# Kernel optimization log

Hardware: AMD Instinct MI355X
Metric: run time of the kernel (lower is better)

## Reference

```python
import jax, jax.numpy as jnp
import numpy as np

B, NX, NY = 16, 1024, 1024
DIN_X, DIN_Y = 768, 283
DK, DV, NH = 80, 80, 8
HK, HV = DK // NH, DV // NH  # 10, 10
NORM = 1.0 / np.sqrt(HK)


def setup_inputs() -> dict:
    key = jax.random.key(0)
    kx, ky, kq, kk, kv = jax.random.split(key, 5)
    x = jax.random.normal(kx, (B, NX, DIN_X), dtype=jnp.float32)
    y = jax.random.normal(ky, (B, NY, DIN_Y), dtype=jnp.float32)
    attn_mask = jnp.zeros((B, NX, NY), dtype=jnp.float32)  # unused in forward (dead arg in original)
    # torch nn.Linear weights are [out, in]; kaiming-uniform-ish init scale
    Wq = jax.random.normal(kq, (DK, DIN_X), dtype=jnp.float32) / np.sqrt(DIN_X)
    Wk = jax.random.normal(kk, (DK, DIN_Y), dtype=jnp.float32) / np.sqrt(DIN_Y)
    Wv = jax.random.normal(kv, (DV, DIN_Y), dtype=jnp.float32) / np.sqrt(DIN_Y)
    return {"x": x, "y": y, "attn_mask": attn_mask, "Wq": Wq, "Wk": Wk, "Wv": Wv}


def reference(x, y, attn_mask, Wq, Wk, Wv):
    b, n_x, _ = x.shape
    n_y = y.shape[1]
    # projections (Linear, no bias): [B,N,D] @ W^T
    q = (x @ Wq.T).reshape(b, n_x, NH, HK).transpose(0, 2, 1, 3)  # [B,H,Nx,hk]
    k = (y @ Wk.T).reshape(b, n_y, NH, HK).transpose(0, 2, 1, 3)  # [B,H,Ny,hk]
    v = (y @ Wv.T).reshape(b, n_y, NH, HV).transpose(0, 2, 1, 3)  # [B,H,Ny,hv]
    scores = jnp.einsum("bhqd,bhkd->bhqk", q, k) * NORM          # [B,H,Nx,Ny]
    dist = jax.nn.softmax(scores, axis=-1)
    # dropout p=0.5 is identity in eval mode
    att = jnp.einsum("bhqk,bhkd->bhqd", dist, v)                  # [B,H,Nx,hv]
    att = att.transpose(0, 2, 1, 3).reshape(b, n_x, DV)           # [B,Nx,dim_v]
    return att, dist
```

## Files before the change

kernel.cpp:

```cpp
#include <hip/hip_runtime.h>
#include <hip/hip_bf16.h>

#define BB 16
#define NXX 1024
#define NYY 1024
#define DINX 768
#define DINY 283
#define NHH 8
#define HKK 10
#define DKV 80
#define NORMF 0.31622776601683794f

__global__ __launch_bounds__(256) void proj_kernel(
    const float* __restrict__ X, const float* __restrict__ W,
    float* __restrict__ Out, int Din) {
  const int LDP = 68;
  __shared__ float Xs[64 * LDP];
  __shared__ float Ws[80 * LDP];
  const int t = threadIdx.x;
  const int rb = blockIdx.x * 64;
  const int tc = t & 15;
  const int tr = t >> 4;

  float acc[4][5];
#pragma unroll
  for (int i = 0; i < 4; ++i)
#pragma unroll
    for (int j = 0; j < 5; ++j) acc[i][j] = 0.f;

  const int nchunk = (Din + 63) >> 6;
  for (int ch = 0; ch < nchunk; ++ch) {
    const int dk = ch << 6;
    __syncthreads();
#pragma unroll
    for (int i = 0; i < 16; ++i) {
      int idx = i * 256 + t;
      int r = idx >> 6, c = idx & 63;
      int d = dk + c;
      Xs[r * LDP + c] = (d < Din) ? X[(size_t)(rb + r) * Din + d] : 0.f;
    }
#pragma unroll
    for (int i = 0; i < 20; ++i) {
      int idx = i * 256 + t;
      int r = idx >> 6, c = idx & 63;
      int d = dk + c;
      Ws[r * LDP + c] = (d < Din) ? W[(size_t)r * Din + d] : 0.f;
    }
    __syncthreads();
#pragma unroll
    for (int dv = 0; dv < 16; ++dv) {
      float4 xv[4], wv[5];
#pragma unroll
      for (int i = 0; i < 4; ++i)
        xv[i] = *(const float4*)&Xs[(tr * 4 + i) * LDP + dv * 4];
#pragma unroll
      for (int j = 0; j < 5; ++j)
        wv[j] = *(const float4*)&Ws[(tc + 16 * j) * LDP + dv * 4];
#pragma unroll
      for (int i = 0; i < 4; ++i)
#pragma unroll
        for (int j = 0; j < 5; ++j) {
          acc[i][j] += xv[i].x * wv[j].x;
          acc[i][j] += xv[i].y * wv[j].y;
          acc[i][j] += xv[i].z * wv[j].z;
          acc[i][j] += xv[i].w * wv[j].w;
        }
    }
  }
#pragma unroll
  for (int i = 0; i < 4; ++i)
#pragma unroll
    for (int j = 0; j < 5; ++j)
      Out[(size_t)(rb + tr * 4 + i) * DKV + tc + 16 * j] = acc[i][j];
}

__global__ __launch_bounds__(256) void attn_kernel(
    const float* __restrict__ Qw, const float* __restrict__ Kw,
    const float* __restrict__ Vw, float* __restrict__ out_att,
    float* __restrict__ out_dist) {
  __shared__ float Ks[256 * 12];
  __shared__ float Vs[256 * 12];
  __shared__ float qs[256 * 12];
  __shared__ float rls[256];

  const int t = threadIdx.x;
  const int bid = blockIdx.x;
  const int qc = bid & 3;
  const int h = (bid >> 2) & 7;
  const int b = bid >> 5;

  const int qrow = qc * 256 + t;
  const size_t g = (size_t)b * NXX + qrow;

  float qr[10];
  {
    const float2* qp = (const float2*)(Qw + g * DKV + h * HKK);
#pragma unroll
    for (int dd = 0; dd < 5; ++dd) {
      float2 v = qp[dd];
      qr[2 * dd] = v.x * NORMF;
      qr[2 * dd + 1] = v.y * NORMF;
      *(float2*)&qs[t * 12 + 2 * dd] = make_float2(qr[2 * dd], qr[2 * dd + 1]);
    }
  }

  float acc[10];
#pragma unroll
  for (int d = 0; d < 10; ++d) acc[d] = 0.f;
  float l = 0.f;

  for (int kt = 0; kt < 4; ++kt) {
    __syncthreads();
    {
      const size_t gk = (size_t)b * NYY + kt * 256 + t;
      const float2* kp = (const float2*)(Kw + gk * DKV + h * HKK);
      const float2* vp = (const float2*)(Vw + gk * DKV + h * HKK);
#pragma unroll
      for (int dd = 0; dd < 5; ++dd) {
        *(float2*)&Ks[t * 12 + 2 * dd] = kp[dd];
        *(float2*)&Vs[t * 12 + 2 * dd] = vp[dd];
      }
    }
    __syncthreads();
#pragma unroll 2
    for (int kk = 0; kk < 256; ++kk) {
      float kf[10], vf[10];
      {
        float4 a0 = *(const float4*)&Ks[kk * 12];
        float4 a1 = *(const float4*)&Ks[kk * 12 + 4];
        float2 a2 = *(const float2*)&Ks[kk * 12 + 8];
        kf[0] = a0.x; kf[1] = a0.y; kf[2] = a0.z; kf[3] = a0.w;
        kf[4] = a1.x; kf[5] = a1.y; kf[6] = a1.z; kf[7] = a1.w;
        kf[8] = a2.x; kf[9] = a2.y;
        float4 b0 = *(const float4*)&Vs[kk * 12];
        float4 b1 = *(const float4*)&Vs[kk * 12 + 4];
        float2 b2 = *(const float2*)&Vs[kk * 12 + 8];
        vf[0] = b0.x; vf[1] = b0.y; vf[2] = b0.z; vf[3] = b0.w;
        vf[4] = b1.x; vf[5] = b1.y; vf[6] = b1.z; vf[7] = b1.w;
        vf[8] = b2.x; vf[9] = b2.y;
      }
      float s = 0.f;
#pragma unroll
      for (int d = 0; d < 10; ++d) s += qr[d] * kf[d];
      float p = __expf(s);
      l += p;
#pragma unroll
      for (int d = 0; d < 10; ++d) acc[d] += p * vf[d];
    }
  }

  const float rl = 1.0f / l;
  rls[t] = rl;
  {
    float* ap = out_att + g * DKV + h * HKK;
#pragma unroll
    for (int dd = 0; dd < 5; ++dd)
      *(float2*)&ap[2 * dd] = make_float2(acc[2 * dd] * rl, acc[2 * dd + 1] * rl);
  }
  __syncthreads();

  const size_t dbase = (((size_t)(b * NHH + h)) * NXX + qc * 256) * NYY;
  for (int kq = 0; kq < 4; ++kq) {
    const int k = kq * 256 + t;
    float kf[10];
    {
      const float2* kp = (const float2*)(Kw + ((size_t)b * NYY + k) * DKV + h * HKK);
#pragma unroll
      for (int dd = 0; dd < 5; ++dd) {
        float2 v = kp[dd];
        kf[2 * dd] = v.x;
        kf[2 * dd + 1] = v.y;
      }
    }
    float* dp = out_dist + dbase + k;
    for (int qq = 0; qq < 256; ++qq) {
      float4 a0 = *(const float4*)&qs[qq * 12];
      float4 a1 = *(const float4*)&qs[qq * 12 + 4];
      float2 a2 = *(const float2*)&qs[qq * 12 + 8];
      float s = kf[0] * a0.x + kf[1] * a0.y + kf[2] * a0.z + kf[3] * a0.w +
                kf[4] * a1.x + kf[5] * a1.y + kf[6] * a1.z + kf[7] * a1.w +
                kf[8] * a2.x + kf[9] * a2.y;
      dp[(size_t)qq * NYY] = __expf(s) * rls[qq];
    }
  }
}

extern "C" void kernel_launch(void* const* d_in, const int* in_sizes, int n_in,
                              void* d_out, int out_size, void* d_ws, size_t ws_size,
                              hipStream_t stream) {
  (void)in_sizes; (void)n_in; (void)out_size; (void)ws_size;
  const float* x = (const float*)d_in[0];
  const float* y = (const float*)d_in[1];
  const float* Wq = (const float*)d_in[3];
  const float* Wk = (const float*)d_in[4];
  const float* Wv = (const float*)d_in[5];

  float* out = (float*)d_out;
  float* att_out = out;
  float* dist_out = out + (size_t)BB * NXX * DKV;

  float* Qw = (float*)d_ws;
  float* Kw = Qw + (size_t)BB * NXX * DKV;
  float* Vw = Kw + (size_t)BB * NYY * DKV;

  proj_kernel<<<256, 256, 0, stream>>>(x, Wq, Qw, DINX);
  proj_kernel<<<256, 256, 0, stream>>>(y, Wk, Kw, DINY);
  proj_kernel<<<256, 256, 0, stream>>>(y, Wv, Vw, DINY);
  attn_kernel<<<BB * NHH * 4, 256, 0, stream>>>(Qw, Kw, Vw, att_out, dist_out);
}
```

Before: 504.1 us.

## Cache softmax probabilities in shared memory and fuse K/V projections

The attention kernel now gives each block 32 query rows with 16 threads per row. It stores the exponentiated scores in a bf16 shared-memory tile, then writes the normalized dist rows with coalesced float4 stores instead of recomputing QK^T and exp in a second pass. The K and V projections are merged into one kernel that reads y once, and the Q projection uses smaller row tiles to launch more blocks. Storing probabilities as bf16 lowers dist precision, and the large shared tile may limit occupancy.

```diff
diff --git a/kernel.cpp b/kernel.cpp
--- a/kernel.cpp
+++ b/kernel.cpp
@@ -11,53 +11,53 @@
 #define DKV 80
 #define NORMF 0.31622776601683794f
 
-__global__ __launch_bounds__(256) void proj_kernel(
-    const float* __restrict__ X, const float* __restrict__ W,
-    float* __restrict__ Out, int Din) {
+#define QT 32
+#define KC 128
+#define SLD 1040
+
+__global__ __launch_bounds__(256) void proj_q_kernel(
+    const float* __restrict__ X, const float* __restrict__ W, float* __restrict__ Out) {
   const int LDP = 68;
-  __shared__ float Xs[64 * LDP];
-  __shared__ float Ws[80 * LDP];
+  __shared__ float Xs[32 * 68];
+  __shared__ float Ws[80 * 68];
   const int t = threadIdx.x;
-  const int rb = blockIdx.x * 64;
+  const int rb = blockIdx.x * 32;
   const int tc = t & 15;
   const int tr = t >> 4;
 
-  float acc[4][5];
-#pragma unroll
-  for (int i = 0; i < 4; ++i)
+  float acc[2][5];
+#pragma unroll
+  for (int i = 0; i < 2; ++i)
 #pragma unroll
     for (int j = 0; j < 5; ++j) acc[i][j] = 0.f;
 
-  const int nchunk = (Din + 63) >> 6;
-  for (int ch = 0; ch < nchunk; ++ch) {
+  for (int ch = 0; ch < 12; ++ch) {
     const int dk = ch << 6;
     __syncthreads();
 #pragma unroll
-    for (int i = 0; i < 16; ++i) {
+    for (int i = 0; i < 8; ++i) {
       int idx = i * 256 + t;
       int r = idx >> 6, c = idx & 63;
-      int d = dk + c;
-      Xs[r * LDP + c] = (d < Din) ? X[(size_t)(rb + r) * Din + d] : 0.f;
+      Xs[r * LDP + c] = X[(size_t)(rb + r) * DINX + dk + c];
     }
 #pragma unroll
     for (int i = 0; i < 20; ++i) {
       int idx = i * 256 + t;
       int r = idx >> 6, c = idx & 63;
-      int d = dk + c;
-      Ws[r * LDP + c] = (d < Din) ? W[(size_t)r * Din + d] : 0.f;
+      Ws[r * LDP + c] = W[(size_t)r * DINX + dk + c];
     }
     __syncthreads();
 #pragma unroll
     for (int dv = 0; dv < 16; ++dv) {
-      float4 xv[4], wv[5];
-#pragma unroll
-      for (int i = 0; i < 4; ++i)
-        xv[i] = *(const float4*)&Xs[(tr * 4 + i) * LDP + dv * 4];
+      float4 xv[2], wv[5];
+#pragma unroll
+      for (int i = 0; i < 2; ++i)
+        xv[i] = *(const float4*)&Xs[(tr * 2 + i) * LDP + dv * 4];
 #pragma unroll
       for (int j = 0; j < 5; ++j)
         wv[j] = *(const float4*)&Ws[(tc + 16 * j) * LDP + dv * 4];
 #pragma unroll
-      for (int i = 0; i < 4; ++i)
+      for (int i = 0; i < 2; ++i)
 #pragma unroll
         for (int j = 0; j < 5; ++j) {
           acc[i][j] += xv[i].x * wv[j].x;
@@ -68,120 +68,180 @@
     }
   }
 #pragma unroll
-  for (int i = 0; i < 4; ++i)
+  for (int i = 0; i < 2; ++i)
 #pragma unroll
     for (int j = 0; j < 5; ++j)
-      Out[(size_t)(rb + tr * 4 + i) * DKV + tc + 16 * j] = acc[i][j];
-}
-
-__global__ __launch_bounds__(256) void attn_kernel(
+      Out[(size_t)(rb + tr * 2 + i) * DKV + tc + 16 * j] = acc[i][j];
+}
+
+__global__ __launch_bounds__(256) void proj_kv_kernel(
+    const float* __restrict__ Y, const float* __restrict__ WK, const float* __restrict__ WV,
+    float* __restrict__ OutK, float* __restrict__ OutV) {
+  const int LDP = 36;
+  __shared__ float Xs[32 * 36];
+  __shared__ float Ws[160 * 36];
+  const int t = threadIdx.x;
+  const int rb = blockIdx.x * 32;
+  const int tc = t & 15;
+  const int tr = t >> 4;
+
+  float acc[2][10];
+#pragma unroll
+  for (int i = 0; i < 2; ++i)
+#pragma unroll
+    for (int j = 0; j < 10; ++j) acc[i][j] = 0.f;
+
+  for (int ch = 0; ch < 9; ++ch) {
+    const int dk = ch << 5;
+    __syncthreads();
+#pragma unroll
+    for (int i = 0; i < 4; ++i) {
+      int idx = i * 256 + t;
+      int r = idx >> 5, c = idx & 31;
+      int d = dk + c;
+      Xs[r * LDP + c] = (d < DINY) ? Y[(size_t)(rb + r) * DINY + d] : 0.f;
+    }
+#pragma unroll
+    for (int i = 0; i < 20; ++i) {
+      int idx = i * 256 + t;
+      int r = idx >> 5, c = idx & 31;
+      int d = dk + c;
+      float v = 0.f;
+      if (d < DINY) v = (r < 80) ? WK[(size_t)r * DINY + d] : WV[(size_t)(r - 80) * DINY + d];
+      Ws[r * LDP + c] = v;
+    }
+    __syncthreads();
+#pragma unroll
+    for (int dv = 0; dv < 8; ++dv) {
+      float4 xv[2], wv[10];
+#pragma unroll
+      for (int i = 0; i < 2; ++i)
+        xv[i] = *(const float4*)&Xs[(tr * 2 + i) * LDP + dv * 4];
+#pragma unroll
+      for (int j = 0; j < 5; ++j) {
+        wv[j] = *(const float4*)&Ws[(tc + 16 * j) * LDP + dv * 4];
+        wv[5 + j] = *(const float4*)&Ws[(80 + tc + 16 * j) * LDP + dv * 4];
+      }
+#pragma unroll
+      for (int i = 0; i < 2; ++i)
+#pragma unroll
+        for (int j = 0; j < 10; ++j) {
+          acc[i][j] += xv[i].x * wv[j].x;
+          acc[i][j] += xv[i].y * wv[j].y;
+          acc[i][j] += xv[i].z * wv[j].z;
+          acc[i][j] += xv[i].w * wv[j].w;
+        }
+    }
+  }
+#pragma unroll
+  for (int i = 0; i < 2; ++i)
+#pragma unroll
+    for (int j = 0; j < 5; ++j) {
+      OutK[(size_t)(rb + tr * 2 + i) * DKV + tc + 16 * j] = acc[i][j];
+      OutV[(size_t)(rb + tr * 2 + i) * DKV + tc + 16 * j] = acc[i][5 + j];
+    }
+}
+
+__global__ __launch_bounds__(512) void attn_kernel(
     const float* __restrict__ Qw, const float* __restrict__ Kw,
     const float* __restrict__ Vw, float* __restrict__ out_att,
     float* __restrict__ out_dist) {
-  __shared__ float Ks[256 * 12];
-  __shared__ float Vs[256 * 12];
-  __shared__ float qs[256 * 12];
-  __shared__ float rls[256];
+  __shared__ __hip_bfloat16 S[QT * SLD];
+  __shared__ float Ks[KC * 12];
+  __shared__ float Vs[KC * 12];
+  __shared__ float rls[QT];
 
   const int t = threadIdx.x;
   const int bid = blockIdx.x;
-  const int qc = bid & 3;
-  const int h = (bid >> 2) & 7;
-  const int b = bid >> 5;
-
-  const int qrow = qc * 256 + t;
-  const size_t g = (size_t)b * NXX + qrow;
+  const int qt = bid & 31;
+  const int h = (bid >> 5) & 7;
+  const int b = bid >> 8;
+
+  const int q = t >> 4;
+  const int kl = t & 15;
+  const int qg = qt * QT + q;
 
   float qr[10];
   {
-    const float2* qp = (const float2*)(Qw + g * DKV + h * HKK);
+    const float2* qp = (const float2*)(Qw + ((size_t)b * NXX + qg) * DKV + h * HKK);
 #pragma unroll
     for (int dd = 0; dd < 5; ++dd) {
       float2 v = qp[dd];
       qr[2 * dd] = v.x * NORMF;
       qr[2 * dd + 1] = v.y * NORMF;
-      *(float2*)&qs[t * 12 + 2 * dd] = make_float2(qr[2 * dd], qr[2 * dd + 1]);
     }
   }
 
   float acc[10];
 #pragma unroll
   for (int d = 0; d < 10; ++d) acc[d] = 0.f;
-  float l = 0.f;
-
-  for (int kt = 0; kt < 4; ++kt) {
-    __syncthreads();
-    {
-      const size_t gk = (size_t)b * NYY + kt * 256 + t;
-      const float2* kp = (const float2*)(Kw + gk * DKV + h * HKK);
-      const float2* vp = (const float2*)(Vw + gk * DKV + h * HKK);
-#pragma unroll
-      for (int dd = 0; dd < 5; ++dd) {
-        *(float2*)&Ks[t * 12 + 2 * dd] = kp[dd];
-        *(float2*)&Vs[t * 12 + 2 * dd] = vp[dd];
-      }
-    }
-    __syncthreads();
+  float lsum = 0.f;
+
+  for (int ch = 0; ch < NYY / KC; ++ch) {
+    __syncthreads();
+    if (t < 2 * KC) {
+      const int r = t & (KC - 1);
+      const float2* src = (const float2*)(((t < KC) ? Kw : Vw) +
+          ((size_t)b * NYY + ch * KC + r) * DKV + h * HKK);
+      float2* dst = (float2*)(((t < KC) ? Ks : Vs) + r * 12);
+#pragma unroll
+      for (int dd = 0; dd < 5; ++dd) dst[dd] = src[dd];
+    }
+    __syncthreads();
+#pragma unroll
+    for (int j = 0; j < KC / 16; ++j) {
+      const int k = (j << 4) + kl;
+      const float* kp = &Ks[k * 12];
+      float4 k0 = *(const float4*)kp;
+      float4 k1 = *(const float4*)(kp + 4);
+      float2 k2 = *(const float2*)(kp + 8);
+      float s = qr[0] * k0.x + qr[1] * k0.y + qr[2] * k0.z + qr[3] * k0.w +
+                qr[4] * k1.x + qr[5] * k1.y + qr[6] * k1.z + qr[7] * k1.w +
+                qr[8] * k2.x + qr[9] * k2.y;
+      float p = __expf(s);
+      lsum += p;
+      const float* vp = &Vs[k * 12];
+      float4 v0 = *(const float4*)vp;
+      float4 v1 = *(const float4*)(vp + 4);
+      float2 v2 = *(const float2*)(vp + 8);
+      acc[0] += p * v0.x; acc[1] += p * v0.y; acc[2] += p * v0.z; acc[3] += p * v0.w;
+      acc[4] += p * v1.x; acc[5] += p * v1.y; acc[6] += p * v1.z; acc[7] += p * v1.w;
+      acc[8] += p * v2.x; acc[9] += p * v2.y;
+      S[q * SLD + (ch << 7) + k] = __float2bfloat16(p);
+    }
+  }
+
+#pragma unroll
+  for (int o = 8; o; o >>= 1) {
+    lsum += __shfl_xor(lsum, o);
+#pragma unroll
+    for (int d = 0; d < 10; ++d) acc[d] += __shfl_xor(acc[d], o);
+  }
+  const float rl = 1.0f / lsum;
+
+  if (kl == 0) {
+    rls[q] = rl;
+    float2* ap = (float2*)(out_att + ((size_t)b * NXX + qg) * DKV + h * HKK);
+#pragma unroll
+    for (int dd = 0; dd < 5; ++dd)
+      ap[dd] = make_float2(acc[2 * dd] * rl, acc[2 * dd + 1] * rl);
+  }
+  __syncthreads();
+
+  const size_t dbase = (((size_t)(b * NHH + h)) * NXX + qt * QT) * NYY;
 #pragma unroll 2
-    for (int kk = 0; kk < 256; ++kk) {
-      float kf[10], vf[10];
-      {
-        float4 a0 = *(const float4*)&Ks[kk * 12];
-        float4 a1 = *(const float4*)&Ks[kk * 12 + 4];
-        float2 a2 = *(const float2*)&Ks[kk * 12 + 8];
-        kf[0] = a0.x; kf[1] = a0.y; kf[2] = a0.z; kf[3] = a0.w;
-        kf[4] = a1.x; kf[5] = a1.y; kf[6] = a1.z; kf[7] = a1.w;
-        kf[8] = a2.x; kf[9] = a2.y;
-        float4 b0 = *(const float4*)&Vs[kk * 12];
-        float4 b1 = *(const float4*)&Vs[kk * 12 + 4];
-        float2 b2 = *(const float2*)&Vs[kk * 12 + 8];
-        vf[0] = b0.x; vf[1] = b0.y; vf[2] = b0.z; vf[3] = b0.w;
-        vf[4] = b1.x; vf[5] = b1.y; vf[6] = b1.z; vf[7] = b1.w;
-        vf[8] = b2.x; vf[9] = b2.y;
-      }
-      float s = 0.f;
-#pragma unroll
-      for (int d = 0; d < 10; ++d) s += qr[d] * kf[d];
-      float p = __expf(s);
-      l += p;
-#pragma unroll
-      for (int d = 0; d < 10; ++d) acc[d] += p * vf[d];
-    }
-  }
-
-  const float rl = 1.0f / l;
-  rls[t] = rl;
-  {
-    float* ap = out_att + g * DKV + h * HKK;
-#pragma unroll
-    for (int dd = 0; dd < 5; ++dd)
-      *(float2*)&ap[2 * dd] = make_float2(acc[2 * dd] * rl, acc[2 * dd + 1] * rl);
-  }
-  __syncthreads();
-
-  const size_t dbase = (((size_t)(b * NHH + h)) * NXX + qc * 256) * NYY;
-  for (int kq = 0; kq < 4; ++kq) {
-    const int k = kq * 256 + t;
-    float kf[10];
-    {
-      const float2* kp = (const float2*)(Kw + ((size_t)b * NYY + k) * DKV + h * HKK);
-#pragma unroll
-      for (int dd = 0; dd < 5; ++dd) {
-        float2 v = kp[dd];
-        kf[2 * dd] = v.x;
-        kf[2 * dd + 1] = v.y;
-      }
-    }
-    float* dp = out_dist + dbase + k;
-    for (int qq = 0; qq < 256; ++qq) {
-      float4 a0 = *(const float4*)&qs[qq * 12];
-      float4 a1 = *(const float4*)&qs[qq * 12 + 4];
-      float2 a2 = *(const float2*)&qs[qq * 12 + 8];
-      float s = kf[0] * a0.x + kf[1] * a0.y + kf[2] * a0.z + kf[3] * a0.w +
-                kf[4] * a1.x + kf[5] * a1.y + kf[6] * a1.z + kf[7] * a1.w +
-                kf[8] * a2.x + kf[9] * a2.y;
-      dp[(size_t)qq * NYY] = __expf(s) * rls[qq];
-    }
+  for (int it = 0; it < 16; ++it) {
+    const int e = it * 2048 + t * 4;
+    const int qq = e >> 10;
+    const int kk = e & 1023;
+    uint2 w = *(const uint2*)&S[qq * SLD + kk];
+    const float rlq = rls[qq];
+    float4 o;
+    o.x = __uint_as_float(w.x << 16) * rlq;
+    o.y = __uint_as_float(w.x & 0xffff0000u) * rlq;
+    o.z = __uint_as_float(w.y << 16) * rlq;
+    o.w = __uint_as_float(w.y & 0xffff0000u) * rlq;
+    *(float4*)(out_dist + dbase + (size_t)qq * NYY + kk) = o;
   }
 }
 
@@ -203,8 +263,7 @@
   float* Kw = Qw + (size_t)BB * NXX * DKV;
   float* Vw = Kw + (size_t)BB * NYY * DKV;
 
-  proj_kernel<<<256, 256, 0, stream>>>(x, Wq, Qw, DINX);
-  proj_kernel<<<256, 256, 0, stream>>>(y, Wk, Kw, DINY);
-  proj_kernel<<<256, 256, 0, stream>>>(y, Wv, Vw, DINY);
-  attn_kernel<<<BB * NHH * 4, 256, 0, stream>>>(Qw, Kw, Vw, att_out, dist_out);
-}
+  proj_q_kernel<<<NXX * BB / 32, 256, 0, stream>>>(x, Wq, Qw);
+  proj_kv_kernel<<<NYY * BB / 32, 256, 0, stream>>>(y, Wk, Wv, Kw, Vw);
+  attn_kernel<<<BB * NHH * 32, 512, 0, stream>>>(Qw, Kw, Vw, att_out, dist_out);
+}
```

New measurement: 463.0 us. 1.09x faster.
